# Kernel tuning notes

Measured on AMD Instinct MI355X. Metric: run time of the kernel, lower is better.

The kernel has to match this reference:

```python
import jax, jax.numpy as jnp
import numpy as np

IN = (16, 16, 16)
OUT = (16, 16, 16)
RT = (8, 8, 8, 8, 8, 8)
RCP = 16
BATCH = 4096


def setup_inputs() -> dict:
    key = jax.random.key(0)
    ks = jax.random.split(key, 14)
    inp = {"x": jax.random.normal(ks[0], (BATCH, int(np.prod(IN))), dtype=jnp.float32)}
    # CP factors of the 6D Tucker core: (rank_tucker_i, rank_cp)
    for i in range(6):
        inp[f"c{i}"] = jax.random.normal(ks[1 + i], (RT[i], RCP), dtype=jnp.float32) * 0.1
    # Tucker factor matrices: out modes then in modes
    dims = list(OUT) + list(IN)
    for i in range(6):
        inp[f"f{i}"] = jax.random.normal(ks[7 + i], (dims[i], RT[i]), dtype=jnp.float32) * 0.1
    inp["bias"] = jnp.zeros((int(np.prod(OUT)),), dtype=jnp.float32)
    return inp


def reference(x, c0, c1, c2, c3, c4, c5, f0, f1, f2, f3, f4, f5, bias):
    # Reconstruct 6D core from its CP factors: (r0,r1,r2,r3,r4,r5)
    core = jnp.einsum('ir,jr,kr,lr,mr,nr->ijklmn', c0, c1, c2, c3, c4, c5)
    # Tucker reconstruction of full weight tensor: (o0,o1,o2,i0,i1,i2)
    W = jnp.einsum('ijklmn,ai,bj,ck,dl,em,fn->abcdef', core, f0, f1, f2, f3, f4, f5)
    x_reshape = x.reshape(-1, *IN)  # (N, i0, i1, i2)
    result = jnp.einsum('abcdef,ndef->nabc', W, x_reshape)  # (N, o0, o1, o2)
    y = result.reshape(-1, int(np.prod(OUT)))
    return y + bias
```

## Files before the change

kernel.cpp:

```cpp
#include <hip/hip_runtime.h>


typedef float f32x4 __attribute__((ext_vector_type(4)));

#define WPB 4

__global__ __launch_bounds__(256, 2)
void kruskal_phase1(const float* __restrict__ x,
                    const float* __restrict__ c3, const float* __restrict__ c4,
                    const float* __restrict__ c5,
                    const float* __restrict__ f3, const float* __restrict__ f4,
                    const float* __restrict__ f5,
                    float* __restrict__ S, int N)
{
    __shared__ __align__(16) float g3t[256];
    __shared__ __align__(16) float g4t[256];
    __shared__ __align__(16) float g5t[256];
    const int tid = threadIdx.x;
    {
        const int i = tid >> 4, r = tid & 15;
        float a3 = 0.f, a4 = 0.f, a5 = 0.f;
#pragma unroll
        for (int k = 0; k < 8; ++k) {
            a3 += f3[i * 8 + k] * c3[k * 16 + r];
            a4 += f4[i * 8 + k] * c4[k * 16 + r];
            a5 += f5[i * 8 + k] * c5[k * 16 + r];
        }
        g3t[i * 16 + r] = a3;
        g4t[r * 16 + i] = a4;
        g5t[r * 16 + i] = a5;
    }
    __syncthreads();

    const int lane = tid & 63, waveId = tid >> 6;
    const int eb  = lane >> 2;
    const int fcb = (lane & 3) * 4;

    f32x4 w1[16];
#pragma unroll
    for (int r = 0; r < 16; ++r)
        w1[r] = (*(const f32x4*)&g5t[r * 16 + fcb]) * g4t[r * 16 + eb];

    const int wgl   = blockIdx.x * WPB + waveId;
    const int total = gridDim.x * WPB;
    for (int n = wgl; n < N; n += total) {
        const float* xn = x + (size_t)n * 4096;
        float s[16];
#pragma unroll
        for (int r = 0; r < 16; ++r) s[r] = 0.f;

#pragma unroll 2
        for (int d = 0; d < 16; ++d) {
            const f32x4 xd = __builtin_nontemporal_load(
                (const f32x4*)(xn + d * 256 + lane * 4));
#pragma unroll
            for (int rq = 0; rq < 4; ++rq) {
                const f32x4 g3q = *(const f32x4*)&g3t[d * 16 + rq * 4];
#pragma unroll
                for (int rr = 0; rr < 4; ++rr) {
                    const int r = rq * 4 + rr;
                    const float p = w1[r].x * xd.x + w1[r].y * xd.y
                                  + w1[r].z * xd.z + w1[r].w * xd.w;
                    s[r] += g3q[rr] * p;
                }
            }
        }

#pragma unroll
        for (int r = 0; r < 16; ++r) {
            float v = s[r];
            v += __shfl_xor(v, 1, 64);
            v += __shfl_xor(v, 2, 64);
            v += __shfl_xor(v, 4, 64);
            v += __shfl_xor(v, 8, 64);
            v += __shfl_xor(v, 16, 64);
            v += __shfl_xor(v, 32, 64);
            s[r] = v;
        }
        float outv = s[0];
#pragma unroll
        for (int r = 1; r < 16; ++r)
            if (lane == r) outv = s[r];
        if (lane < 16)
            S[(size_t)n * 16 + lane] = outv;
    }
}

__global__ __launch_bounds__(256, 2)
void kruskal_phase2(const float* __restrict__ S,
                    const float* __restrict__ c0, const float* __restrict__ c1,
                    const float* __restrict__ c2,
                    const float* __restrict__ f0, const float* __restrict__ f1,
                    const float* __restrict__ f2,
                    const float* __restrict__ bias,
                    float* __restrict__ out, int N)
{
    __shared__ __align__(16) float g0t[256];
    __shared__ __align__(16) float g1t[256];
    __shared__ __align__(16) float g2t[256];
    const int tid = threadIdx.x;
    {
        const int i = tid >> 4, r = tid & 15;
        float a0 = 0.f, a1 = 0.f, a2 = 0.f;
#pragma unroll
        for (int k = 0; k < 8; ++k) {
            a0 += f0[i * 8 + k] * c0[k * 16 + r];
            a1 += f1[i * 8 + k] * c1[k * 16 + r];
            a2 += f2[i * 8 + k] * c2[k * 16 + r];
        }
        g0t[r * 16 + i] = a0;
        g1t[r * 16 + i] = a1;
        g2t[r * 16 + i] = a2;
    }
    __syncthreads();

    const int lane = tid & 63, waveId = tid >> 6;
    const int eb  = lane >> 2;
    const int fcb = (lane & 3) * 4;

    const int wgl    = blockIdx.x * WPB + waveId;
    const int chunk  = wgl & 15;
    const int slot   = wgl >> 4;
    const int stride = (gridDim.x * WPB) >> 4;

    f32x4 w[16];
#pragma unroll
    for (int r = 0; r < 16; ++r)
        w[r] = (*(const f32x4*)&g2t[r * 16 + fcb])
             * (g0t[r * 16 + chunk] * g1t[r * 16 + eb]);
    const f32x4 bv = *(const f32x4*)(bias + chunk * 256 + lane * 4);

#pragma unroll 1
    for (int n = slot; n < N; n += stride) {
        const f32x4* Sr = (const f32x4*)(S + (size_t)n * 16);
        const f32x4 s0 = Sr[0], s1 = Sr[1], s2 = Sr[2], s3 = Sr[3];
        f32x4 acc = bv;
        acc += s0.x * w[0];  acc += s0.y * w[1];
        acc += s0.z * w[2];  acc += s0.w * w[3];
        acc += s1.x * w[4];  acc += s1.y * w[5];
        acc += s1.z * w[6];  acc += s1.w * w[7];
        acc += s2.x * w[8];  acc += s2.y * w[9];
        acc += s2.z * w[10]; acc += s2.w * w[11];
        acc += s3.x * w[12]; acc += s3.y * w[13];
        acc += s3.z * w[14]; acc += s3.w * w[15];
        __builtin_nontemporal_store(
            acc, (f32x4*)(out + (size_t)n * 4096 + chunk * 256 + lane * 4));
    }
}

extern "C" void kernel_launch(void* const* d_in, const int* in_sizes, int n_in,
                              void* d_out, int out_size, void* d_ws, size_t ws_size,
                              hipStream_t stream) {
    const float* x  = (const float*)d_in[0];
    const float* c0 = (const float*)d_in[1];
    const float* c1 = (const float*)d_in[2];
    const float* c2 = (const float*)d_in[3];
    const float* c3 = (const float*)d_in[4];
    const float* c4 = (const float*)d_in[5];
    const float* c5 = (const float*)d_in[6];
    const float* f0 = (const float*)d_in[7];
    const float* f1 = (const float*)d_in[8];
    const float* f2 = (const float*)d_in[9];
    const float* f3 = (const float*)d_in[10];
    const float* f4 = (const float*)d_in[11];
    const float* f5 = (const float*)d_in[12];
    const float* bias = (const float*)d_in[13];
    float* out = (float*)d_out;
    float* S   = (float*)d_ws;

    const int N = in_sizes[0] / 4096;

    kruskal_phase1<<<dim3(1024), dim3(256), 0, stream>>>(
        x, c3, c4, c5, f3, f4, f5, S, N);
    kruskal_phase2<<<dim3(1024), dim3(256), 0, stream>>>(
        S, c0, c1, c2, f0, f1, f2, bias, out, N);
}
```

Baseline: 152.6 us.

## Fuse CP projection and output expansion into a single kernel

Merges the two phases into one kernel: each wave computes the 16 rank coefficients for a sample, then immediately expands them into the 4096-wide output, with the bias staged in shared memory. This removes the second kernel launch and the round trip of the intermediate S buffer through global memory. In exchange, each wave now holds two sets of 16 vector weights in registers (more register pressure at launch_bounds 256,2). LDS use also grows by about 22KB per block, and output writes are now serialized after the reduction within each wave rather than spread across separate waves.

```diff
diff --git a/kernel.cpp b/kernel.cpp
--- a/kernel.cpp
+++ b/kernel.cpp
@@ -6,29 +6,49 @@
 #define WPB 4
 
 __global__ __launch_bounds__(256, 2)
-void kruskal_phase1(const float* __restrict__ x,
-                    const float* __restrict__ c3, const float* __restrict__ c4,
-                    const float* __restrict__ c5,
-                    const float* __restrict__ f3, const float* __restrict__ f4,
-                    const float* __restrict__ f5,
-                    float* __restrict__ S, int N)
+void kruskal_fused(const float* __restrict__ x,
+                   const float* __restrict__ c0, const float* __restrict__ c1,
+                   const float* __restrict__ c2, const float* __restrict__ c3,
+                   const float* __restrict__ c4, const float* __restrict__ c5,
+                   const float* __restrict__ f0, const float* __restrict__ f1,
+                   const float* __restrict__ f2, const float* __restrict__ f3,
+                   const float* __restrict__ f4, const float* __restrict__ f5,
+                   const float* __restrict__ bias,
+                   float* __restrict__ out, int N)
 {
     __shared__ __align__(16) float g3t[256];
     __shared__ __align__(16) float g4t[256];
     __shared__ __align__(16) float g5t[256];
+    __shared__ __align__(16) float g0c[256];
+    __shared__ __align__(16) float g1t[256];
+    __shared__ __align__(16) float g2t[256];
+    __shared__ __align__(16) float bsh[4096];
+
     const int tid = threadIdx.x;
     {
         const int i = tid >> 4, r = tid & 15;
-        float a3 = 0.f, a4 = 0.f, a5 = 0.f;
+        float a0 = 0.f, a1 = 0.f, a2 = 0.f, a3 = 0.f, a4 = 0.f, a5 = 0.f;
 #pragma unroll
         for (int k = 0; k < 8; ++k) {
+            a0 += f0[i * 8 + k] * c0[k * 16 + r];
+            a1 += f1[i * 8 + k] * c1[k * 16 + r];
+            a2 += f2[i * 8 + k] * c2[k * 16 + r];
             a3 += f3[i * 8 + k] * c3[k * 16 + r];
             a4 += f4[i * 8 + k] * c4[k * 16 + r];
             a5 += f5[i * 8 + k] * c5[k * 16 + r];
         }
+        g0c[i * 16 + r] = a0;
+        g1t[r * 16 + i] = a1;
+        g2t[r * 16 + i] = a2;
         g3t[i * 16 + r] = a3;
         g4t[r * 16 + i] = a4;
         g5t[r * 16 + i] = a5;
+    }
+    {
+        const f32x4* b4 = (const f32x4*)bias;
+        f32x4* bs4 = (f32x4*)bsh;
+#pragma unroll
+        for (int j = 0; j < 4; ++j) bs4[j * 256 + tid] = b4[j * 256 + tid];
     }
     __syncthreads();
 
@@ -36,15 +56,18 @@
     const int eb  = lane >> 2;
     const int fcb = (lane & 3) * 4;
 
-    f32x4 w1[16];
+    f32x4 w1[16], wb[16];
 #pragma unroll
-    for (int r = 0; r < 16; ++r)
+    for (int r = 0; r < 16; ++r) {
         w1[r] = (*(const f32x4*)&g5t[r * 16 + fcb]) * g4t[r * 16 + eb];
+        wb[r] = (*(const f32x4*)&g2t[r * 16 + fcb]) * g1t[r * 16 + eb];
+    }
 
     const int wgl   = blockIdx.x * WPB + waveId;
     const int total = gridDim.x * WPB;
     for (int n = wgl; n < N; n += total) {
         const float* xn = x + (size_t)n * 4096;
+
         float s[16];
 #pragma unroll
         for (int r = 0; r < 16; ++r) s[r] = 0.f;
@@ -77,74 +100,23 @@
             v += __shfl_xor(v, 32, 64);
             s[r] = v;
         }
-        float outv = s[0];
+
+        float* on = out + (size_t)n * 4096;
+#pragma unroll 2
+        for (int a = 0; a < 16; ++a) {
+            f32x4 acc = *(const f32x4*)&bsh[a * 256 + lane * 4];
 #pragma unroll
-        for (int r = 1; r < 16; ++r)
-            if (lane == r) outv = s[r];
-        if (lane < 16)
-            S[(size_t)n * 16 + lane] = outv;
-    }
-}
-
-__global__ __launch_bounds__(256, 2)
-void kruskal_phase2(const float* __restrict__ S,
-                    const float* __restrict__ c0, const float* __restrict__ c1,
-                    const float* __restrict__ c2,
-                    const float* __restrict__ f0, const float* __restrict__ f1,
-                    const float* __restrict__ f2,
-                    const float* __restrict__ bias,
-                    float* __restrict__ out, int N)
-{
-    __shared__ __align__(16) float g0t[256];
-    __shared__ __align__(16) float g1t[256];
-    __shared__ __align__(16) float g2t[256];
-    const int tid = threadIdx.x;
-    {
-        const int i = tid >> 4, r = tid & 15;
-        float a0 = 0.f, a1 = 0.f, a2 = 0.f;
+            for (int rq = 0; rq < 4; ++rq) {
+                const f32x4 g0q = *(const f32x4*)&g0c[a * 16 + rq * 4];
 #pragma unroll
-        for (int k = 0; k < 8; ++k) {
-            a0 += f0[i * 8 + k] * c0[k * 16 + r];
-            a1 += f1[i * 8 + k] * c1[k * 16 + r];
-            a2 += f2[i * 8 + k] * c2[k * 16 + r];
+                for (int rr = 0; rr < 4; ++rr) {
+                    const int r = rq * 4 + rr;
+                    acc += (s[r] * g0q[rr]) * wb[r];
+                }
+            }
+            __builtin_nontemporal_store(
+                acc, (f32x4*)(on + a * 256 + lane * 4));
         }
-        g0t[r * 16 + i] = a0;
-        g1t[r * 16 + i] = a1;
-        g2t[r * 16 + i] = a2;
-    }
-    __syncthreads();
-
-    const int lane = tid & 63, waveId = tid >> 6;
-    const int eb  = lane >> 2;
-    const int fcb = (lane & 3) * 4;
-
-    const int wgl    = blockIdx.x * WPB + waveId;
-    const int chunk  = wgl & 15;
-    const int slot   = wgl >> 4;
-    const int stride = (gridDim.x * WPB) >> 4;
-
-    f32x4 w[16];
-#pragma unroll
-    for (int r = 0; r < 16; ++r)
-        w[r] = (*(const f32x4*)&g2t[r * 16 + fcb])
-             * (g0t[r * 16 + chunk] * g1t[r * 16 + eb]);
-    const f32x4 bv = *(const f32x4*)(bias + chunk * 256 + lane * 4);
-
-#pragma unroll 1
-    for (int n = slot; n < N; n += stride) {
-        const f32x4* Sr = (const f32x4*)(S + (size_t)n * 16);
-        const f32x4 s0 = Sr[0], s1 = Sr[1], s2 = Sr[2], s3 = Sr[3];
-        f32x4 acc = bv;
-        acc += s0.x * w[0];  acc += s0.y * w[1];
-        acc += s0.z * w[2];  acc += s0.w * w[3];
-        acc += s1.x * w[4];  acc += s1.y * w[5];
-        acc += s1.z * w[6];  acc += s1.w * w[7];
-        acc += s2.x * w[8];  acc += s2.y * w[9];
-        acc += s2.z * w[10]; acc += s2.w * w[11];
-        acc += s3.x * w[12]; acc += s3.y * w[13];
-        acc += s3.z * w[14]; acc += s3.w * w[15];
-        __builtin_nontemporal_store(
-            acc, (f32x4*)(out + (size_t)n * 4096 + chunk * 256 + lane * 4));
     }
 }
 
@@ -166,12 +138,10 @@
     const float* f5 = (const float*)d_in[12];
     const float* bias = (const float*)d_in[13];
     float* out = (float*)d_out;
-    float* S   = (float*)d_ws;
+    (void)d_ws; (void)ws_size;
 
     const int N = in_sizes[0] / 4096;
 
-    kruskal_phase1<<<dim3(1024), dim3(256), 0, stream>>>(
-        x, c3, c4, c5, f3, f4, f5, S, N);
-    kruskal_phase2<<<dim3(1024), dim3(256), 0, stream>>>(
-        S, c0, c1, c2, f0, f1, f2, bias, out, N);
+    kruskal_fused<<<dim3(1024), dim3(256), 0, stream>>>(
+        x, c0, c1, c2, c3, c4, c5, f0, f1, f2, f3, f4, f5, bias, out, N);
 }
```

Result: faster. 149.2 us (-2.3%).
